# Kernel tuning notes

Hardware: AMD Instinct MI355X
Metric: run time of the kernel (lower is better)

## Reference

```python
import jax, jax.numpy as jnp
import numpy as np

KNN_K = 10        # init kwarg knn_k
EPS_COS = 1e-8    # torch F.cosine_similarity default eps
EPS_SCALE = 1e-6  # clamp on median displacement variance


def _knn_indices(pts, k):
    """pts: [B, P, 3]. Returns [B, P, k] indices of nearest points.

    Matches torch: topk over negative squared pairwise distance (self point
    has distance 0 and is therefore included among the neighbors).
    """
    inner = jnp.einsum('bpd,bqd->bpq', pts, pts)            # [B,P,P]
    xx = jnp.sum(pts * pts, axis=-1)                        # [B,P]
    neg_dist = 2.0 * inner - xx[:, :, None] - xx[:, None, :]
    return jax.lax.top_k(neg_dist, k)[1]                    # [B,P,k]


def setup_inputs() -> dict:
    key = jax.random.key(0)
    k1, k2 = jax.random.split(key)
    B, D, T, P = 4, 128, 8, 4096
    return {
        'encoded': jax.random.normal(k1, (B, D, T * P), dtype=jnp.float32),
        'points_4d': jax.random.normal(k2, (B, T, P, 4), dtype=jnp.float32),
        'num_frames': T,
        'pts_per_frame': P,
    }


def reference(encoded, points_4d, num_frames, pts_per_frame):
    B, D, _ = encoded.shape
    xyz = points_4d[..., :3]                                # [B,T,P,3]
    feat = encoded.reshape(B, D, num_frames, pts_per_frame)
    k = min(KNN_K, pts_per_frame - 1)
    gather = jax.vmap(lambda a, i: a[i])                    # per-batch fancy gather

    total = jnp.asarray(0.0, dtype=encoded.dtype)
    for t in range(num_frames - 1):                         # small fixed frame loop
        pts = xyz[:, t]                                     # [B,P,3]
        disp = xyz[:, t + 1] - pts                          # [B,P,3]
        idx = _knn_indices(pts, k)                          # [B,P,k]

        nbr_disp = gather(disp, idx)                        # [B,P,k,3]
        disp_diff = nbr_disp - disp[:, :, None, :]
        disp_var = jnp.mean(jnp.sum(disp_diff * disp_diff, axis=-1), axis=-1)  # [B,P]

        # torch .median() on even-length returns the lower middle element
        flat = jnp.sort(disp_var.reshape(-1))
        scale = jnp.maximum(flat[(flat.shape[0] - 1) // 2], EPS_SCALE)
        rigidity = jax.lax.stop_gradient(jnp.exp(-disp_var / scale))  # detached

        feat_t = jnp.transpose(feat[:, :, t], (0, 2, 1))    # [B,P,D]
        nbr_feat = gather(feat_t, idx)                      # [B,P,k,D]
        num = jnp.einsum('bpd,bpkd->bpk', feat_t, nbr_feat)
        nq = jnp.maximum(jnp.linalg.norm(feat_t, axis=-1), EPS_COS)   # [B,P]
        nn_ = jnp.maximum(jnp.linalg.norm(nbr_feat, axis=-1), EPS_COS)  # [B,P,k]
        cos_sim = num / (nq[:, :, None] * nn_)
        mean_sim = jnp.mean(cos_sim, axis=-1)               # [B,P]

        total = total + jnp.mean(rigidity * (1.0 - mean_sim))
    return total / max(num_frames - 1, 1)
```

## Files before the change

kernel.cpp:

```cpp
#include <hip/hip_runtime.h>
#include <math.h>

#define BB 4
#define DD 128
#define TT 8
#define PP 4096
#define KK 10
#define NT 7
#define BP (BB*PP)
#define NQ (NT*BP)
#define NBLK_COS 896
#define QPB 128

#define CHUNKS 4
#define CSZ (PP/CHUNKS)
#define FCAP 12

#define OFF_FEATT 0u
#define OFF_PARTV 0u
#define OFF_CAND4 20971520u
#define OFF_TAU   23068672u
#define OFF_FCNT  23527424u
#define OFF_FLIST 25362432u
#define OFF_IDX   58720256u
#define OFF_DV    63307776u
#define OFF_NORM  63766528u
#define OFF_SCALE 64225280u
#define OFF_PART  64225536u

typedef __fp16 f16x2 __attribute__((ext_vector_type(2)));
union H2U { f16x2 h; unsigned u; };

__device__ __forceinline__ f16x2 pk_min(f16x2 a, f16x2 b) {
  f16x2 d;
  asm("v_pk_min_f16 %0, %1, %2" : "=v"(d) : "v"(a), "v"(b));
  return d;
}
__device__ __forceinline__ f16x2 pk_max(f16x2 a, f16x2 b) {
  f16x2 d;
  asm("v_pk_max_f16 %0, %1, %2" : "=v"(d) : "v"(a), "v"(b));
  return d;
}

__device__ __forceinline__ float md_of(const float4 q, const float4 c) {
  float s = q.w + c.w;
  float inner = fmaf(q.x, c.x, fmaf(q.y, c.y, q.z * c.z));
  return fmaf(-2.0f, inner, s);
}

__device__ __forceinline__ void ins2(f16x2 (&bv)[KK], float mdA, float mdB) {
  H2U cv;
  cv.h = __builtin_amdgcn_cvt_pkrtz(mdA, mdB);
  cv.u += 0x00020002u;
  bv[KK - 1] = pk_min(bv[KK - 1], cv.h);
#pragma unroll
  for (int i = KK - 1; i > 0; --i) {
    f16x2 lo = pk_min(bv[i - 1], bv[i]);
    f16x2 hi = pk_max(bv[i - 1], bv[i]);
    bv[i - 1] = lo;
    bv[i] = hi;
  }
}
__device__ __forceinline__ void insh(f16x2 (&bv)[KK], f16x2 h) {
  bv[KK - 1] = pk_min(bv[KK - 1], h);
#pragma unroll
  for (int i = KK - 1; i > 0; --i) {
    f16x2 lo = pk_min(bv[i - 1], bv[i]);
    f16x2 hi = pk_max(bv[i - 1], bv[i]);
    bv[i - 1] = lo;
    bv[i] = hi;
  }
}

__device__ __forceinline__ void insf(float (&bv)[KK], float v) {
  bv[KK - 1] = fminf(bv[KK - 1], v);
#pragma unroll
  for (int i = KK - 1; i > 0; --i) {
    float lo = fminf(bv[i - 1], bv[i]);
    float hi = fmaxf(bv[i - 1], bv[i]);
    bv[i - 1] = lo;
    bv[i] = hi;
  }
}

__device__ __forceinline__ void insp(float (&v)[KK], int (&vi)[KK], float md,
                                     int j) {
  bool en = md < v[KK - 1];
  v[KK - 1] = en ? md : v[KK - 1];
  vi[KK - 1] = en ? j : vi[KK - 1];
#pragma unroll
  for (int i = KK - 1; i > 0; --i) {
    bool sw = v[i] < v[i - 1];
    float tv = sw ? v[i - 1] : v[i];
    v[i - 1] = sw ? v[i] : v[i - 1];
    v[i] = tv;
    int ti = sw ? vi[i - 1] : vi[i];
    vi[i - 1] = sw ? vi[i] : vi[i - 1];
    vi[i] = ti;
  }
}

__device__ __forceinline__ void rec12(int (&a)[FCAP], int cnt, int j) {
#pragma unroll
  for (int r = 0; r < FCAP; ++r) a[r] = (cnt == r) ? j : a[r];
}

__global__ __launch_bounds__(256) void prep_cand(
    const float* __restrict__ pts4, float4* __restrict__ cand4) {
  const int i = blockIdx.x * 256 + threadIdx.x;
  float4 v = ((const float4*)pts4)[i];
  v.w = fmaf(v.x, v.x, fmaf(v.y, v.y, v.z * v.z));
  cand4[i] = v;
}

__global__ __launch_bounds__(256) void knn_thr_partial(
    const float4* __restrict__ cand4, unsigned* __restrict__ part) {
  const int qg = blockIdx.x >> 2;
  const int c = blockIdx.x & 3;
  const int b = blockIdx.y, t = blockIdx.z;
  const float4* __restrict__ src = cand4 + ((size_t)(b * TT + t) * PP);
  const float4* __restrict__ ch = src + c * CSZ;

  const int p = qg * 256 + threadIdx.x;
  const float4 q = src[p];

  H2U inf2;
  inf2.u = 0x7C007C00u;
  f16x2 l1[KK], l2[KK];
#pragma unroll
  for (int i = 0; i < KK; ++i) { l1[i] = inf2.h; l2[i] = inf2.h; }

  for (int j = 0; j < CSZ; j += 4) {
    float4 c0 = ch[j], c1 = ch[j + 1], c2 = ch[j + 2], c3 = ch[j + 3];
    float md0 = md_of(q, c0);
    float md1 = md_of(q, c1);
    float md2 = md_of(q, c2);
    float md3 = md_of(q, c3);
    ins2(l1, md0, md1);
    ins2(l2, md2, md3);
  }
#pragma unroll
  for (int r = 0; r < KK; ++r) insh(l1, l2[r]);

  const size_t qid = (size_t)(t * BB + b) * PP + p;
#pragma unroll
  for (int r = 0; r < KK; ++r) {
    H2U w;
    w.h = l1[r];
    part[(size_t)(c * KK + r) * NQ + qid] = w.u;
  }
}

__global__ __launch_bounds__(256) void tau_kernel(
    const unsigned* __restrict__ part, float* __restrict__ tau_arr) {
  const int g = blockIdx.x * 256 + threadIdx.x;
  float bv[KK];
#pragma unroll
  for (int i = 0; i < KK; ++i) bv[i] = INFINITY;
#pragma unroll
  for (int c = 0; c < CHUNKS; ++c) {
#pragma unroll
    for (int r = 0; r < KK; ++r) {
      H2U w;
      w.u = part[(size_t)(c * KK + r) * NQ + g];
      insf(bv, (float)w.h.x);
      insf(bv, (float)w.h.y);
    }
  }
  tau_arr[g] = bv[KK - 1] + 1e-4f;
}

__global__ __launch_bounds__(256) void knn_filter(
    const float4* __restrict__ cand4, const float* __restrict__ tau_arr,
    unsigned* __restrict__ fcnt, unsigned short* __restrict__ flist) {
  const int qg = blockIdx.x >> 2;
  const int c = blockIdx.x & 3;
  const int b = blockIdx.y, t = blockIdx.z;
  const float4* __restrict__ src = cand4 + ((size_t)(b * TT + t) * PP);
  const float4* __restrict__ ch = src + c * CSZ;
  const int jbase = c * CSZ;

  const int p = qg * 256 + threadIdx.x;
  const size_t g = (size_t)(t * BB + b) * PP + p;
  const float4 q = src[p];
  const float tau = tau_arr[g];

  int sel[FCAP];
#pragma unroll
  for (int r = 0; r < FCAP; ++r) sel[r] = 0;
  int cnt = 0;

  for (int j = 0; j < CSZ; j += 8) {
    float4 c0 = ch[j], c1 = ch[j + 1], c2 = ch[j + 2], c3 = ch[j + 3];
    float4 c4 = ch[j + 4], c5 = ch[j + 5], c6 = ch[j + 6], c7 = ch[j + 7];
    float m0 = md_of(q, c0), m1 = md_of(q, c1), m2 = md_of(q, c2),
          m3 = md_of(q, c3);
    float m4 = md_of(q, c4), m5 = md_of(q, c5), m6 = md_of(q, c6),
          m7 = md_of(q, c7);
#define FLT(mm, jj)                                         \
    if ((mm) <= tau) { rec12(sel, cnt, jbase + (jj)); ++cnt; }
    FLT(m0, j); FLT(m1, j + 1); FLT(m2, j + 2); FLT(m3, j + 3);
    FLT(m4, j + 4); FLT(m5, j + 5); FLT(m6, j + 6); FLT(m7, j + 7);
#undef FLT
  }

  fcnt[(size_t)c * NQ + g] = (unsigned)cnt;
#pragma unroll
  for (int r = 0; r < FCAP; ++r)
    flist[(size_t)(c * FCAP + r) * NQ + g] = (unsigned short)sel[r];
}

__global__ __launch_bounds__(256) void knn_finish(
    const float4* __restrict__ cand4, const float* __restrict__ pts4,
    const unsigned* __restrict__ fcnt, const unsigned short* __restrict__ flist,
    int* __restrict__ idx_out, float* __restrict__ dv_out) {
  const int g = blockIdx.x * 256 + threadIdx.x;
  const int t = g >> 14;
  const int rem = g & (BP - 1);
  const int b = rem >> 12;
  const int p = rem & (PP - 1);
  const float4* __restrict__ src = cand4 + ((size_t)(b * TT + t) * PP);
  const float4* __restrict__ src1 =
      (const float4*)pts4 + ((size_t)(b * TT + t + 1) * PP);

  const float4 q = src[p];

  float v[KK];
  int vi[KK];
#pragma unroll
  for (int i = 0; i < KK; ++i) { v[i] = INFINITY; vi[i] = 0; }

#pragma unroll
  for (int c = 0; c < CHUNKS; ++c) {
    int cn = (int)fcnt[(size_t)c * NQ + g];
    cn = cn < FCAP ? cn : FCAP;
#pragma unroll
    for (int r = 0; r < FCAP; ++r) {
      if (r < cn) {
        int j = (int)flist[(size_t)(c * FCAP + r) * NQ + g];
        insp(v, vi, md_of(q, src[j]), j);
      }
    }
  }

  float4 a1 = src1[p];
  const float dqx = a1.x - q.x, dqy = a1.y - q.y, dqz = a1.z - q.z;
  float s = 0.0f;
  int* myidx = idx_out + (size_t)g * KK;
#pragma unroll
  for (int r = 0; r < KK; ++r) {
    int j = vi[r];
    float4 cc = src[j];
    float4 n1 = src1[j];
    float dx = (n1.x - cc.x) - dqx;
    float dy = (n1.y - cc.y) - dqy;
    float dz = (n1.z - cc.z) - dqz;
    s += fmaf(dx, dx, fmaf(dy, dy, dz * dz));
    myidx[r] = j;
  }
  dv_out[g] = s * (1.0f / KK);
}

__global__ __launch_bounds__(256) void transpose_kernel(
    const float* __restrict__ encoded, float* __restrict__ featT) {
  __shared__ float tile[32][33];
  const int slice = blockIdx.z;
  const int t = slice / BB, b = slice % BB;
  const int p0 = blockIdx.x * 32, d0 = blockIdx.y * 32;
  const int tx = threadIdx.x, ty = threadIdx.y;
#pragma unroll
  for (int r = 0; r < 4; ++r) {
    int d = d0 + ty + r * 8;
    tile[ty + r * 8][tx] =
        encoded[((size_t)(b * DD + d)) * (TT * PP) + (size_t)t * PP + p0 + tx];
  }
  __syncthreads();
#pragma unroll
  for (int r = 0; r < 4; ++r) {
    int p = p0 + ty + r * 8;
    featT[((size_t)slice * PP + p) * DD + d0 + tx] = tile[tx][ty + r * 8];
  }
}

__global__ __launch_bounds__(256) void norms_kernel(
    const float* __restrict__ featT, float* __restrict__ norms) {
  const int w = threadIdx.x >> 6, lane = threadIdx.x & 63;
  const int wid = blockIdx.x * 4 + w;
  for (int i = 0; i < 32; ++i) {
    const int g = wid * 32 + i;
    float2 f = *(const float2*)(featT + (size_t)g * DD + lane * 2);
    float part = fmaf(f.x, f.x, f.y * f.y);
#pragma unroll
    for (int o = 32; o > 0; o >>= 1) part += __shfl_xor(part, o);
    if (lane == 0) norms[g] = sqrtf(part);
  }
}

__global__ __launch_bounds__(256) void median_kernel(
    const float* __restrict__ disp_var, float* __restrict__ scale) {
  const int t = blockIdx.x;
  const unsigned* u = (const unsigned*)(disp_var + (size_t)t * BP);
  __shared__ unsigned hist[256];
  __shared__ unsigned sh_prefix;
  __shared__ int sh_rank;
  if (threadIdx.x == 0) { sh_prefix = 0u; sh_rank = (BP - 1) >> 1; }
  __syncthreads();
  for (int pass = 0; pass < 4; ++pass) {
    const int shift = 24 - pass * 8;
    hist[threadIdx.x] = 0u;
    __syncthreads();
    const unsigned hmask = (pass == 0) ? 0u : (0xFFFFFFFFu << (shift + 8));
    const unsigned prefix = sh_prefix;
    for (int i = threadIdx.x; i < BP; i += 256) {
      unsigned v = u[i];
      if ((v & hmask) == prefix) atomicAdd(&hist[(v >> shift) & 255u], 1u);
    }
    __syncthreads();
    if (threadIdx.x == 0) {
      int rank = sh_rank;
      unsigned run = 0u;
      for (int c = 0; c < 256; ++c) {
        unsigned h = hist[c];
        if (run + h > (unsigned)rank) {
          sh_rank = rank - (int)run;
          sh_prefix = prefix | ((unsigned)c << shift);
          break;
        }
        run += h;
      }
    }
    __syncthreads();
  }
  if (threadIdx.x == 0) {
    float med = __uint_as_float(sh_prefix);
    scale[t] = fmaxf(med, 1e-6f);
  }
}

__global__ __launch_bounds__(256) void cos_loss_kernel(
    const float* __restrict__ featT, const int* __restrict__ idxw,
    const float* __restrict__ norms, const float* __restrict__ dv,
    const float* __restrict__ scale, float* __restrict__ partial) {
  const int w = threadIdx.x >> 6, lane = threadIdx.x & 63;
  __shared__ float wsum[4];
  float acc = 0.0f;
  const int qbase = blockIdx.x * QPB + w * (QPB / 4);
  for (int i = 0; i < QPB / 4; ++i) {
    const int g = qbase + i;
    const int t = g >> 14;
    const int p = g & (PP - 1);
    const int slice = g - p;
    const float* fbase = featT + (size_t)g * DD;
    float2 fq = *(const float2*)(fbase + lane * 2);
    float nq = fmaxf(norms[g], 1e-8f);
    const int* ip = idxw + (size_t)g * KK;
    float msum = 0.0f;
#pragma unroll
    for (int k = 0; k < KK; ++k) {
      int j = ip[k];
      const float* nb = featT + (size_t)(slice + j) * DD;
      float2 fn = *(const float2*)(nb + lane * 2);
      float part = fmaf(fq.x, fn.x, fq.y * fn.y);
#pragma unroll
      for (int o = 32; o > 0; o >>= 1) part += __shfl_xor(part, o);
      float nn = fmaxf(norms[slice + j], 1e-8f);
      msum += part / (nq * nn);
    }
    float mean_sim = msum * (1.0f / KK);
    float rig = expf(-dv[g] / scale[t]);
    acc += rig * (1.0f - mean_sim);
  }
  if (lane == 0) wsum[w] = acc;
  __syncthreads();
  if (threadIdx.x == 0)
    partial[blockIdx.x] = (wsum[0] + wsum[1]) + (wsum[2] + wsum[3]);
}

__global__ __launch_bounds__(256) void final_reduce_kernel(
    const float* __restrict__ partial, float* __restrict__ out) {
  __shared__ float sh[256];
  float s = 0.0f;
  for (int i = threadIdx.x; i < NBLK_COS; i += 256) s += partial[i];
  sh[threadIdx.x] = s;
  __syncthreads();
  for (int st = 128; st > 0; st >>= 1) {
    if (threadIdx.x < st) sh[threadIdx.x] += sh[threadIdx.x + st];
    __syncthreads();
  }
  if (threadIdx.x == 0) out[0] = sh[0] * (1.0f / (float)NQ);
}

extern "C" void kernel_launch(void* const* d_in, const int* in_sizes, int n_in,
                              void* d_out, int out_size, void* d_ws,
                              size_t ws_size, hipStream_t stream) {
  const float* encoded = (const float*)d_in[0];
  const float* pts4 = (const float*)d_in[1];
  char* ws = (char*)d_ws;
  float* featT = (float*)(ws + OFF_FEATT);
  unsigned* part = (unsigned*)(ws + OFF_PARTV);
  float4* cand4 = (float4*)(ws + OFF_CAND4);
  float* tau_arr = (float*)(ws + OFF_TAU);
  unsigned* fcnt = (unsigned*)(ws + OFF_FCNT);
  unsigned short* flist = (unsigned short*)(ws + OFF_FLIST);
  int* idxw = (int*)(ws + OFF_IDX);
  float* dv = (float*)(ws + OFF_DV);
  float* norms = (float*)(ws + OFF_NORM);
  float* scale = (float*)(ws + OFF_SCALE);
  float* partial = (float*)(ws + OFF_PART);
  float* outp = (float*)d_out;

  prep_cand<<<(BB * TT * PP) / 256, 256, 0, stream>>>(pts4, cand4);
  knn_thr_partial<<<dim3(16 * CHUNKS, BB, NT), 256, 0, stream>>>(cand4, part);
  tau_kernel<<<NQ / 256, 256, 0, stream>>>(part, tau_arr);
  knn_filter<<<dim3(16 * CHUNKS, BB, NT), 256, 0, stream>>>(cand4, tau_arr,
                                                            fcnt, flist);
  knn_finish<<<NQ / 256, 256, 0, stream>>>(cand4, pts4, fcnt, flist, idxw, dv);
  transpose_kernel<<<dim3(PP / 32, DD / 32, NT * BB), dim3(32, 8), 0, stream>>>(
      encoded, featT);
  norms_kernel<<<NBLK_COS, 256, 0, stream>>>(featT, norms);
  median_kernel<<<NT, 256, 0, stream>>>(dv, scale);
  cos_loss_kernel<<<NBLK_COS, 256, 0, stream>>>(featT, idxw, norms, dv, scale,
                                                partial);
  final_reduce_kernel<<<1, 256, 0, stream>>>(partial, outp);
}
```

Baseline: 676.4 us.

## Estimate KNN threshold from candidate subset, LDS filter lists, overflow fallback

The threshold pass now scans only the first 256 candidates of each chunk, 1024 points in all instead of the full set. This cuts that pass's distance work by four, at the cost of a looser per-query threshold that lets more candidates through. The filter records survivors in a per-thread shared-memory list with a larger cap of 28. This replaces the predicated register-select chain and so avoids the register cost of a bigger cap. The finish kernel walks the variable-length lists with runtime loops and rescans a whole chunk against the threshold whenever it overflowed. That keeps results exact, but it adds more insertion work per query and a divergent slow path.

```diff
diff --git a/kernel.cpp b/kernel.cpp
--- a/kernel.cpp
+++ b/kernel.cpp
@@ -14,7 +14,9 @@
 
 #define CHUNKS 4
 #define CSZ (PP/CHUNKS)
-#define FCAP 12
+#define TSZ 256
+#define FCAP 28
+#define LSTRIDE (FCAP+1)
 
 #define OFF_FEATT 0u
 #define OFF_PARTV 0u
@@ -100,11 +102,6 @@
   }
 }
 
-__device__ __forceinline__ void rec12(int (&a)[FCAP], int cnt, int j) {
-#pragma unroll
-  for (int r = 0; r < FCAP; ++r) a[r] = (cnt == r) ? j : a[r];
-}
-
 __global__ __launch_bounds__(256) void prep_cand(
     const float* __restrict__ pts4, float4* __restrict__ cand4) {
   const int i = blockIdx.x * 256 + threadIdx.x;
@@ -119,7 +116,7 @@
   const int c = blockIdx.x & 3;
   const int b = blockIdx.y, t = blockIdx.z;
   const float4* __restrict__ src = cand4 + ((size_t)(b * TT + t) * PP);
-  const float4* __restrict__ ch = src + c * CSZ;
+  const float4* __restrict__ ch = src + c * TSZ;
 
   const int p = qg * 256 + threadIdx.x;
   const float4 q = src[p];
@@ -130,7 +127,7 @@
 #pragma unroll
   for (int i = 0; i < KK; ++i) { l1[i] = inf2.h; l2[i] = inf2.h; }
 
-  for (int j = 0; j < CSZ; j += 4) {
+  for (int j = 0; j < TSZ; j += 4) {
     float4 c0 = ch[j], c1 = ch[j + 1], c2 = ch[j + 2], c3 = ch[j + 3];
     float md0 = md_of(q, c0);
     float md1 = md_of(q, c1);
@@ -173,23 +170,22 @@
 __global__ __launch_bounds__(256) void knn_filter(
     const float4* __restrict__ cand4, const float* __restrict__ tau_arr,
     unsigned* __restrict__ fcnt, unsigned short* __restrict__ flist) {
+  __shared__ unsigned slds[256 * LSTRIDE];
   const int qg = blockIdx.x >> 2;
   const int c = blockIdx.x & 3;
   const int b = blockIdx.y, t = blockIdx.z;
   const float4* __restrict__ src = cand4 + ((size_t)(b * TT + t) * PP);
   const float4* __restrict__ ch = src + c * CSZ;
   const int jbase = c * CSZ;
-
-  const int p = qg * 256 + threadIdx.x;
+  const int tid = threadIdx.x;
+
+  const int p = qg * 256 + tid;
   const size_t g = (size_t)(t * BB + b) * PP + p;
   const float4 q = src[p];
   const float tau = tau_arr[g];
-
-  int sel[FCAP];
-#pragma unroll
-  for (int r = 0; r < FCAP; ++r) sel[r] = 0;
+  unsigned* my = slds + tid * LSTRIDE;
+
   int cnt = 0;
-
   for (int j = 0; j < CSZ; j += 8) {
     float4 c0 = ch[j], c1 = ch[j + 1], c2 = ch[j + 2], c3 = ch[j + 3];
     float4 c4 = ch[j + 4], c5 = ch[j + 5], c6 = ch[j + 6], c7 = ch[j + 7];
@@ -197,23 +193,27 @@
           m3 = md_of(q, c3);
     float m4 = md_of(q, c4), m5 = md_of(q, c5), m6 = md_of(q, c6),
           m7 = md_of(q, c7);
-#define FLT(mm, jj)                                         \
-    if ((mm) <= tau) { rec12(sel, cnt, jbase + (jj)); ++cnt; }
+#define FLT(mm, jj)                                             \
+    if ((mm) <= tau) {                                          \
+      if (cnt < FCAP) my[cnt] = (unsigned)(jbase + (jj));       \
+      ++cnt;                                                    \
+    }
     FLT(m0, j); FLT(m1, j + 1); FLT(m2, j + 2); FLT(m3, j + 3);
     FLT(m4, j + 4); FLT(m5, j + 5); FLT(m6, j + 6); FLT(m7, j + 7);
 #undef FLT
   }
 
   fcnt[(size_t)c * NQ + g] = (unsigned)cnt;
-#pragma unroll
+#pragma unroll 4
   for (int r = 0; r < FCAP; ++r)
-    flist[(size_t)(c * FCAP + r) * NQ + g] = (unsigned short)sel[r];
+    flist[(size_t)(c * FCAP + r) * NQ + g] = (unsigned short)my[r];
 }
 
 __global__ __launch_bounds__(256) void knn_finish(
     const float4* __restrict__ cand4, const float* __restrict__ pts4,
-    const unsigned* __restrict__ fcnt, const unsigned short* __restrict__ flist,
-    int* __restrict__ idx_out, float* __restrict__ dv_out) {
+    const float* __restrict__ tau_arr, const unsigned* __restrict__ fcnt,
+    const unsigned short* __restrict__ flist, int* __restrict__ idx_out,
+    float* __restrict__ dv_out) {
   const int g = blockIdx.x * 256 + threadIdx.x;
   const int t = g >> 14;
   const int rem = g & (BP - 1);
@@ -224,21 +224,25 @@
       (const float4*)pts4 + ((size_t)(b * TT + t + 1) * PP);
 
   const float4 q = src[p];
+  const float tau = tau_arr[g];
 
   float v[KK];
   int vi[KK];
 #pragma unroll
   for (int i = 0; i < KK; ++i) { v[i] = INFINITY; vi[i] = 0; }
 
-#pragma unroll
   for (int c = 0; c < CHUNKS; ++c) {
-    int cn = (int)fcnt[(size_t)c * NQ + g];
-    cn = cn < FCAP ? cn : FCAP;
-#pragma unroll
-    for (int r = 0; r < FCAP; ++r) {
-      if (r < cn) {
+    const int cn = (int)fcnt[(size_t)c * NQ + g];
+    if (cn <= FCAP) {
+      for (int r = 0; r < cn; ++r) {
         int j = (int)flist[(size_t)(c * FCAP + r) * NQ + g];
         insp(v, vi, md_of(q, src[j]), j);
+      }
+    } else {
+      const float4* chb = src + c * CSZ;
+      for (int jj = 0; jj < CSZ; ++jj) {
+        float mdv = md_of(q, chb[jj]);
+        if (mdv <= tau) insp(v, vi, mdv, c * CSZ + jj);
       }
     }
   }
@@ -414,7 +418,8 @@
   tau_kernel<<<NQ / 256, 256, 0, stream>>>(part, tau_arr);
   knn_filter<<<dim3(16 * CHUNKS, BB, NT), 256, 0, stream>>>(cand4, tau_arr,
                                                             fcnt, flist);
-  knn_finish<<<NQ / 256, 256, 0, stream>>>(cand4, pts4, fcnt, flist, idxw, dv);
+  knn_finish<<<NQ / 256, 256, 0, stream>>>(cand4, pts4, tau_arr, fcnt, flist,
+                                           idxw, dv);
   transpose_kernel<<<dim3(PP / 32, DD / 32, NT * BB), dim3(32, 8), 0, stream>>>(
       encoded, featT);
   norms_kernel<<<NBLK_COS, 256, 0, stream>>>(featT, norms);
```

Measured after the change: 990.6 us. +46.4%, slower.
